# Kernel optimization log

Measured on AMD Instinct MI355X. Metric: run time of the kernel, lower is better.

## Reference

```python
import jax, jax.numpy as jnp
import numpy as np

N_NODES = 100000
N_EDGES = 640000
IN_DIM = 128
# PyG SAGEConv pyramid per SageCox(num_layers=4)
DIMS = [128, 85, 56, 28, 1]  # 85=int(128*2/3), 56=int(85*2/3), 28=int(56/2)


def setup_inputs() -> dict:
    key = jax.random.key(0)
    ks = jax.random.split(key, 2 + 3 * 4)
    inp = {
        "x": jax.random.normal(ks[0], (N_NODES, IN_DIM), dtype=jnp.float32),
        "edge_index": jax.random.randint(ks[1], (2, N_EDGES), 0, N_NODES, dtype=jnp.int64),
    }
    # Per-layer params: lin_l (weight+bias, applied to aggregated neighbors),
    # lin_r (weight only, applied to root features) -- PyG SAGEConv defaults.
    for i in range(4):
        din, dout = DIMS[i], DIMS[i + 1]
        inp[f"Wl{i}"] = jax.random.normal(ks[2 + 3 * i], (din, dout), dtype=jnp.float32) * 0.05
        inp[f"bl{i}"] = jax.random.normal(ks[3 + 3 * i], (dout,), dtype=jnp.float32) * 0.05
        inp[f"Wr{i}"] = jax.random.normal(ks[4 + 3 * i], (din, dout), dtype=jnp.float32) * 0.05
    return inp


def _sage_layer(x, src, dst, Wl, bl, Wr):
    # mean aggregation of source-node features at destination nodes
    msg = x[src]                                            # [E, din] gather
    agg = jax.ops.segment_sum(msg, dst, num_segments=N_NODES)
    deg = jax.ops.segment_sum(jnp.ones((src.shape[0],), x.dtype), dst,
                              num_segments=N_NODES)
    mean = agg / jnp.maximum(deg, 1.0)[:, None]             # [N, din]
    return mean @ Wl + bl + x @ Wr                          # [N, dout]


def reference(x, edge_index, Wl0, bl0, Wr0, Wl1, bl1, Wr1, Wl2, bl2, Wr2, Wl3, bl3, Wr3):
    src, dst = edge_index[0], edge_index[1]
    params = [(Wl0, bl0, Wr0), (Wl1, bl1, Wr1), (Wl2, bl2, Wr2), (Wl3, bl3, Wr3)]
    for Wl, bl, Wr in params:
        x = _sage_layer(x, src, dst, Wl, bl, Wr)
    return x  # [N, 1] risk scores
```

## Files before the change

### kernel.cpp

```cpp
#include <hip/hip_runtime.h>


#define NNODES 100000
#define NEDGES 640000

using bf16x8 = __attribute__((ext_vector_type(8))) short;
using f32x4  = __attribute__((ext_vector_type(4))) float;

__device__ __forceinline__ unsigned short f2bf(float f) {
    union { float f; unsigned u; } v; v.f = f;
    unsigned r = v.u + 0x7fffu + ((v.u >> 16) & 1u);
    return (unsigned short)(r >> 16);
}
__device__ __forceinline__ float bf2f(unsigned b) {
    union { unsigned u; float f; } v; v.u = b << 16;
    return v.f;
}


__global__ void hist_kernel(const int* __restrict__ edst, int* __restrict__ deg, int E) {
    int i = blockIdx.x * blockDim.x + threadIdx.x;
    if (i < E) atomicAdd(&deg[edst[i]], 1);
}

__global__ void scanA_kernel(const int* __restrict__ deg, int* __restrict__ bsum, int N) {
    __shared__ int s[256];
    int i = blockIdx.x * 256 + threadIdx.x;
    s[threadIdx.x] = (i < N) ? deg[i] : 0;
    __syncthreads();
    for (int off = 128; off > 0; off >>= 1) {
        if (threadIdx.x < off) s[threadIdx.x] += s[threadIdx.x + off];
        __syncthreads();
    }
    if (threadIdx.x == 0) bsum[blockIdx.x] = s[0];
}

__global__ void scanB_kernel(const int* __restrict__ bsum, int* __restrict__ bpre, int nb) {
    __shared__ int s[512];
    int t = threadIdx.x;
    int v = (t < nb) ? bsum[t] : 0;
    s[t] = v;
    __syncthreads();
    for (int off = 1; off < 512; off <<= 1) {
        int add = (t >= off) ? s[t - off] : 0;
        __syncthreads();
        s[t] += add;
        __syncthreads();
    }
    if (t < nb) bpre[t] = s[t] - v;
}

__global__ void scanC_kernel(const int* __restrict__ deg, const int* __restrict__ bpre,
                             int* __restrict__ rowptr, int* __restrict__ cursor, int N, int E) {
    __shared__ int s[256];
    int t = threadIdx.x;
    int i = blockIdx.x * 256 + t;
    int v = (i < N) ? deg[i] : 0;
    s[t] = v;
    __syncthreads();
    for (int off = 1; off < 256; off <<= 1) {
        int add = (t >= off) ? s[t - off] : 0;
        __syncthreads();
        s[t] += add;
        __syncthreads();
    }
    if (i < N) {
        int excl = bpre[blockIdx.x] + s[t] - v;
        rowptr[i] = excl;
        cursor[i] = excl;
        if (i == N - 1) rowptr[N] = E;
    }
}

__global__ void fill_kernel(const int* __restrict__ esrc, const int* __restrict__ edst,
                            int* __restrict__ cursor, int* __restrict__ csr, int E) {
    int i = blockIdx.x * blockDim.x + threadIdx.x;
    if (i < E) {
        int pos = atomicAdd(&cursor[edst[i]], 1);
        csr[pos] = esrc[i];
    }
}


__device__ __forceinline__ void packT_one(const float* Wl, const float* Wr,
                                          unsigned short* WcT, int idx, int DIN,
                                          int KP, int DOUT, int DOUTP) {
    int c = idx / KP, k = idx - c * KP;
    float v = 0.0f;
    if (k < DIN) {
        if (c < DOUT) v = Wl[k * DOUT + c];
        else if (c >= DOUTP && c < DOUTP + DOUT) v = Wr[k * DOUT + (c - DOUTP)];
    }
    WcT[idx] = f2bf(v);
}

__global__ void packAll_kernel(const float* __restrict__ Wl0, const float* __restrict__ Wr0,
                               const float* __restrict__ Wl1, const float* __restrict__ Wr1,
                               const float* __restrict__ Wl2, const float* __restrict__ Wr2,
                               unsigned short* __restrict__ Wc0,
                               unsigned short* __restrict__ Wc1,
                               unsigned short* __restrict__ Wc2) {
    const int S0 = 176 * 128, S1 = 112 * 96, S2 = 64 * 64;
    int idx = blockIdx.x * blockDim.x + threadIdx.x;
    if (idx < S0) packT_one(Wl0, Wr0, Wc0, idx, 128, 128, 85, 85);
    else if (idx < S0 + S1) packT_one(Wl1, Wr1, Wc1, idx - S0, 85, 96, 56, 56);
    else if (idx < S0 + S1 + S2) packT_one(Wl2, Wr2, Wc2, idx - S0 - S1, 56, 64, 28, 28);
}


template <bool XFP32, int KP, int SIN, int NTILES, int DOUT, int DOUTP, int SPP, int SACC>
__global__ void __launch_bounds__(256)
projm_kernel(const void* __restrict__ xin,
             const unsigned short* __restrict__ WcT,
             const float* __restrict__ bl,
             unsigned short* __restrict__ p,
             unsigned short* __restrict__ acc_out, int N) {
    constexpr int KT = KP / 32;
    const int lane = threadIdx.x & 63;
    const int wave = threadIdx.x >> 6;
    const int l15 = lane & 15;
    const int lk  = lane >> 4;

    const int row0 = (blockIdx.x * 4 + wave) * 32;

    bf16x8 afrag[2][KT];
#pragma unroll
    for (int h = 0; h < 2; ++h) {
        int arow = row0 + h * 16 + l15;
        if (arow >= N) arow = N - 1;
        if constexpr (XFP32) {
            const float* xr = (const float*)xin + (size_t)arow * SIN + lk * 8;
#pragma unroll
            for (int kt = 0; kt < KT; ++kt) {
                const float4 a = *(const float4*)(xr + kt * 32);
                const float4 b = *(const float4*)(xr + kt * 32 + 4);
                bf16x8 v;
                v[0] = (short)f2bf(a.x); v[1] = (short)f2bf(a.y);
                v[2] = (short)f2bf(a.z); v[3] = (short)f2bf(a.w);
                v[4] = (short)f2bf(b.x); v[5] = (short)f2bf(b.y);
                v[6] = (short)f2bf(b.z); v[7] = (short)f2bf(b.w);
                afrag[h][kt] = v;
            }
        } else {
            const unsigned short* xr = (const unsigned short*)xin + (size_t)arow * SIN + lk * 8;
#pragma unroll
            for (int kt = 0; kt < KT; ++kt)
                afrag[h][kt] = *(const bf16x8*)(xr + kt * 32);
        }
    }

#pragma unroll 2
    for (int nt = 0; nt < NTILES; ++nt) {
        const unsigned short* wp = WcT + (size_t)(nt * 16 + l15) * KP + lk * 8;
        bf16x8 bfrag[KT];
#pragma unroll
        for (int kt = 0; kt < KT; ++kt)
            bfrag[kt] = *(const bf16x8*)(wp + kt * 32);

        f32x4 a0 = {0.f, 0.f, 0.f, 0.f};
        f32x4 a1 = {0.f, 0.f, 0.f, 0.f};
#pragma unroll
        for (int kt = 0; kt < KT; ++kt) {
            a0 = __builtin_amdgcn_mfma_f32_16x16x32_bf16(afrag[0][kt], bfrag[kt], a0, 0, 0, 0);
            a1 = __builtin_amdgcn_mfma_f32_16x16x32_bf16(afrag[1][kt], bfrag[kt], a1, 0, 0, 0);
        }

        const int col = nt * 16 + l15;
#pragma unroll
        for (int h = 0; h < 2; ++h) {
            const f32x4 a = h ? a1 : a0;
            const int rbase = row0 + h * 16 + lk * 4;
#pragma unroll
            for (int j = 0; j < 4; ++j) {
                const int row = rbase + j;
                if (row >= N) continue;
                const float v = a[j];
                if (col < DOUT) {
                    p[(size_t)row * SPP + col] = f2bf(v);
                } else if (col >= DOUTP && col < DOUTP + DOUT) {
                    const int co = col - DOUTP;
                    acc_out[(size_t)row * SACC + co] = f2bf(v + bl[co]);
                }
            }
        }
    }
}


template <int DOUT, int SP, int SN>
__global__ void __launch_bounds__(256)
gatherb_kernel(const int* __restrict__ rowptr, const int* __restrict__ csr,
               const unsigned short* __restrict__ p, const unsigned short* __restrict__ acc,
               unsigned short* __restrict__ xnext, int N) {
    const int node = __builtin_amdgcn_readfirstlane((blockIdx.x * 256 + threadIdx.x) >> 6);
    const int lane = threadIdx.x & 63;
    if (node >= N) return;
    const int beg = rowptr[node], end = rowptr[node + 1];
    const float inv = 1.0f / (float)max(end - beg, 1);
    constexpr int NPAIR = (DOUT + 1) / 2;
    const int co = 2 * lane;

    float s0 = 0.f, s1 = 0.f, s2 = 0.f, s3 = 0.f;
    float h0 = 0.f, h1 = 0.f, h2 = 0.f, h3 = 0.f;
    if (lane < NPAIR) {
        int j = beg;
        for (; j + 4 <= end; j += 4) {
            const unsigned u0 = *(const unsigned*)(p + (size_t)csr[j]     * SP + co);
            const unsigned u1 = *(const unsigned*)(p + (size_t)csr[j + 1] * SP + co);
            const unsigned u2 = *(const unsigned*)(p + (size_t)csr[j + 2] * SP + co);
            const unsigned u3 = *(const unsigned*)(p + (size_t)csr[j + 3] * SP + co);
            s0 += bf2f(u0 & 0xffffu); h0 += bf2f(u0 >> 16);
            s1 += bf2f(u1 & 0xffffu); h1 += bf2f(u1 >> 16);
            s2 += bf2f(u2 & 0xffffu); h2 += bf2f(u2 >> 16);
            s3 += bf2f(u3 & 0xffffu); h3 += bf2f(u3 >> 16);
        }
        for (; j < end; ++j) {
            const unsigned u0 = *(const unsigned*)(p + (size_t)csr[j] * SP + co);
            s0 += bf2f(u0 & 0xffffu); h0 += bf2f(u0 >> 16);
        }
    }
    if (co < SN) {
        const float slo = (s0 + s1) + (s2 + s3);
        const float shi = (h0 + h1) + (h2 + h3);
        float lo = 0.f, hi = 0.f;
        if (co < DOUT)     lo = bf2f((unsigned)acc[(size_t)node * SP + co])     + inv * slo;
        if (co + 1 < DOUT) hi = bf2f((unsigned)acc[(size_t)node * SP + co + 1]) + inv * shi;
        const unsigned w = (unsigned)f2bf(lo) | ((unsigned)f2bf(hi) << 16);
        *(unsigned*)(xnext + (size_t)node * SN + co) = w;
    }
}


__global__ void __launch_bounds__(256)
gather2g_kernel(const int* __restrict__ rowptr, const int* __restrict__ csr,
                const unsigned short* __restrict__ p, const unsigned short* __restrict__ acc,
                const float* __restrict__ Wl3, const float* __restrict__ bl3,
                const float* __restrict__ Wr3,
                float* __restrict__ p3, float* __restrict__ out, int N) {
    const int node = __builtin_amdgcn_readfirstlane((blockIdx.x * 256 + threadIdx.x) >> 6);
    const int lane = threadIdx.x & 63;
    if (node >= N) return;
    const int beg = rowptr[node], end = rowptr[node + 1];
    const float inv = 1.0f / (float)max(end - beg, 1);
    const int co = 2 * lane;

    float s0 = 0.f, s1 = 0.f, s2 = 0.f, s3 = 0.f;
    float h0 = 0.f, h1 = 0.f, h2 = 0.f, h3 = 0.f;
    if (lane < 14) {
        int j = beg;
        for (; j + 4 <= end; j += 4) {
            const unsigned u0 = *(const unsigned*)(p + (size_t)csr[j]     * 32 + co);
            const unsigned u1 = *(const unsigned*)(p + (size_t)csr[j + 1] * 32 + co);
            const unsigned u2 = *(const unsigned*)(p + (size_t)csr[j + 2] * 32 + co);
            const unsigned u3 = *(const unsigned*)(p + (size_t)csr[j + 3] * 32 + co);
            s0 += bf2f(u0 & 0xffffu); h0 += bf2f(u0 >> 16);
            s1 += bf2f(u1 & 0xffffu); h1 += bf2f(u1 >> 16);
            s2 += bf2f(u2 & 0xffffu); h2 += bf2f(u2 >> 16);
            s3 += bf2f(u3 & 0xffffu); h3 += bf2f(u3 >> 16);
        }
        for (; j < end; ++j) {
            const unsigned u0 = *(const unsigned*)(p + (size_t)csr[j] * 32 + co);
            s0 += bf2f(u0 & 0xffffu); h0 += bf2f(u0 >> 16);
        }
    }
    float xlo = 0.f, xhi = 0.f, wl0 = 0.f, wl1 = 0.f, wr0 = 0.f, wr1 = 0.f;
    if (lane < 14) {
        xlo = bf2f((unsigned)acc[(size_t)node * 32 + co])     + inv * ((s0 + s1) + (s2 + s3));
        xhi = bf2f((unsigned)acc[(size_t)node * 32 + co + 1]) + inv * ((h0 + h1) + (h2 + h3));
        wl0 = Wl3[co]; wl1 = Wl3[co + 1];
        wr0 = Wr3[co]; wr1 = Wr3[co + 1];
    }
    float sl = xlo * wl0 + xhi * wl1;
    float sr = xlo * wr0 + xhi * wr1;
#pragma unroll
    for (int off = 32; off > 0; off >>= 1) {
        sl += __shfl_xor(sl, off, 64);
        sr += __shfl_xor(sr, off, 64);
    }
    if (lane == 0) {
        p3[node] = sl;
        out[node] = sr + bl3[0];
    }
}

__global__ void gather1_kernel(const int* __restrict__ rowptr, const int* __restrict__ csr,
                               const float* __restrict__ p, float* __restrict__ out, int N) {
    const int node = blockIdx.x * blockDim.x + threadIdx.x;
    if (node >= N) return;
    const int beg = rowptr[node], end = rowptr[node + 1];
    const float inv = 1.0f / (float)max(end - beg, 1);
    float a0 = 0.f, a1 = 0.f, a2 = 0.f, a3 = 0.f;
    int j = beg;
    for (; j + 4 <= end; j += 4) {
        a0 += p[csr[j]]; a1 += p[csr[j + 1]]; a2 += p[csr[j + 2]]; a3 += p[csr[j + 3]];
    }
    for (; j < end; ++j) a0 += p[csr[j]];
    out[node] += inv * ((a0 + a1) + (a2 + a3));
}


extern "C" void kernel_launch(void* const* d_in, const int* in_sizes, int n_in,
                              void* d_out, int out_size, void* d_ws, size_t ws_size,
                              hipStream_t stream) {
    const float* x  = (const float*)d_in[0];
    const int*   ei = (const int*)d_in[1];
    const int N = NNODES;
    const int E = NEDGES;
    const int* esrc = ei;
    const int* edst = ei + E;

    const float* Wl[4] = {(const float*)d_in[2], (const float*)d_in[5],
                          (const float*)d_in[8], (const float*)d_in[11]};
    const float* bl[4] = {(const float*)d_in[3], (const float*)d_in[6],
                          (const float*)d_in[9], (const float*)d_in[12]};
    const float* Wr[4] = {(const float*)d_in[4], (const float*)d_in[7],
                          (const float*)d_in[10], (const float*)d_in[13]};

    char* base = (char*)d_ws;
    size_t off = 0;
    auto alloc = [&](size_t bytes) {
        char* r = base + off;
        off += (bytes + 255) & ~(size_t)255;
        return r;
    };
    unsigned short* pB   = (unsigned short*)alloc((size_t)N * 96 * 2);
    unsigned short* accB = (unsigned short*)alloc((size_t)N * 96 * 2);
    unsigned short* xp   = (unsigned short*)alloc((size_t)N * 96 * 2);
    float*          p3   = (float*)alloc((size_t)N * 4);
    unsigned short* Wc0  = (unsigned short*)alloc((size_t)176 * 128 * 2);
    unsigned short* Wc1  = (unsigned short*)alloc((size_t)112 * 96 * 2);
    unsigned short* Wc2  = (unsigned short*)alloc((size_t)64 * 64 * 2);
    int* degi   = (int*)alloc((size_t)N * 4);
    int* rowptr = (int*)alloc((size_t)(N + 1) * 4);
    int* cursor = (int*)alloc((size_t)N * 4);
    int* csr    = (int*)alloc((size_t)E * 4);
    int* bsum   = (int*)alloc(512 * 4);
    int* bpre   = (int*)alloc(512 * 4);

    unsigned short* x2 = xp;

    const int nb = (N + 255) / 256;

    hipMemsetAsync(degi, 0, (size_t)N * sizeof(int), stream);
    hist_kernel<<<(E + 255) / 256, 256, 0, stream>>>(edst, degi, E);
    scanA_kernel<<<nb, 256, 0, stream>>>(degi, bsum, N);
    scanB_kernel<<<1, 512, 0, stream>>>(bsum, bpre, nb);
    scanC_kernel<<<nb, 256, 0, stream>>>(degi, bpre, rowptr, cursor, N, E);
    fill_kernel<<<(E + 255) / 256, 256, 0, stream>>>(esrc, edst, cursor, csr, E);

    const int packTot = 176 * 128 + 112 * 96 + 64 * 64;
    packAll_kernel<<<(packTot + 255) / 256, 256, 0, stream>>>(
        Wl[0], Wr[0], Wl[1], Wr[1], Wl[2], Wr[2], Wc0, Wc1, Wc2);

    const int projBlocks = (N + 127) / 128;

    projm_kernel<true, 128, 128, 11, 85, 85, 96, 96><<<projBlocks, 256, 0, stream>>>(
        x, Wc0, bl[0], pB, accB, N);
    gatherb_kernel<85, 96, 96><<<(N + 3) / 4, 256, 0, stream>>>(
        rowptr, csr, pB, accB, xp, N);

    projm_kernel<false, 96, 96, 7, 56, 56, 64, 64><<<projBlocks, 256, 0, stream>>>(
        xp, Wc1, bl[1], pB, accB, N);
    gatherb_kernel<56, 64, 64><<<(N + 3) / 4, 256, 0, stream>>>(
        rowptr, csr, pB, accB, x2, N);

    projm_kernel<false, 64, 64, 4, 28, 28, 32, 32><<<projBlocks, 256, 0, stream>>>(
        x2, Wc2, bl[2], pB, accB, N);

    gather2g_kernel<<<(N + 3) / 4, 256, 0, stream>>>(
        rowptr, csr, pB, accB, Wl[3], bl[3], Wr[3], p3, (float*)d_out, N);
    gather1_kernel<<<(N + 255) / 256, 256, 0, stream>>>(
        rowptr, csr, p3, (float*)d_out, N);
}
```

Baseline: 268.5 us.

## Stage weights and outputs through LDS for coalesced projection stores

The projection kernel now copies the packed weight matrix into shared memory once per block and reads MFMA B-fragments from there instead of global memory. Output tiles are written to an LDS staging buffer and then stored with 16-byte vectorized, fully coalesced writes, replacing scattered 2-byte per-element stores. The weight packing is padded so the Wl and Wr halves each fill exactly SPP columns, and padded columns now receive zeros. This adds LDS usage and extra block barriers, which may lower occupancy.

```diff
diff --git a/kernel.cpp b/kernel.cpp
--- a/kernel.cpp
+++ b/kernel.cpp
@@ -100,33 +100,48 @@
                                unsigned short* __restrict__ Wc0,
                                unsigned short* __restrict__ Wc1,
                                unsigned short* __restrict__ Wc2) {
-    const int S0 = 176 * 128, S1 = 112 * 96, S2 = 64 * 64;
+    const int S0 = 192 * 128, S1 = 128 * 96, S2 = 64 * 64;
     int idx = blockIdx.x * blockDim.x + threadIdx.x;
-    if (idx < S0) packT_one(Wl0, Wr0, Wc0, idx, 128, 128, 85, 85);
-    else if (idx < S0 + S1) packT_one(Wl1, Wr1, Wc1, idx - S0, 85, 96, 56, 56);
-    else if (idx < S0 + S1 + S2) packT_one(Wl2, Wr2, Wc2, idx - S0 - S1, 56, 64, 28, 28);
-}
-
-
-template <bool XFP32, int KP, int SIN, int NTILES, int DOUT, int DOUTP, int SPP, int SACC>
+    if (idx < S0) packT_one(Wl0, Wr0, Wc0, idx, 128, 128, 85, 96);
+    else if (idx < S0 + S1) packT_one(Wl1, Wr1, Wc1, idx - S0, 85, 96, 56, 64);
+    else if (idx < S0 + S1 + S2) packT_one(Wl2, Wr2, Wc2, idx - S0 - S1, 56, 64, 28, 32);
+}
+
+
+template <bool XFP32, int KP, int SIN, int NTILES, int DOUT, int SPP>
 __global__ void __launch_bounds__(256)
 projm_kernel(const void* __restrict__ xin,
              const unsigned short* __restrict__ WcT,
              const float* __restrict__ bl,
              unsigned short* __restrict__ p,
              unsigned short* __restrict__ acc_out, int N) {
-    constexpr int KT = KP / 32;
+    constexpr int KT   = KP / 32;
+    constexpr int HT   = NTILES / 2;
+    constexpr int CW   = NTILES * 16;
+    constexpr int WSTR = KP + 8;
+    constexpr int LSTR = SPP + 8;
+    static_assert(HT * 16 == SPP, "phase width must equal SPP");
+    __shared__ short wS[CW * WSTR];
+    __shared__ short oS[128 * LSTR];
+
     const int lane = threadIdx.x & 63;
     const int wave = threadIdx.x >> 6;
     const int l15 = lane & 15;
     const int lk  = lane >> 4;
-
-    const int row0 = (blockIdx.x * 4 + wave) * 32;
+    const int row0 = blockIdx.x * 128;
+    const int wrow = wave * 32;
+
+    for (int c8 = threadIdx.x; c8 < CW * (KP / 8); c8 += 256) {
+        const int c  = c8 / (KP / 8);
+        const int k8 = c8 - c * (KP / 8);
+        *(bf16x8*)(wS + c * WSTR + k8 * 8) =
+            *(const bf16x8*)(WcT + (size_t)c * KP + k8 * 8);
+    }
 
     bf16x8 afrag[2][KT];
 #pragma unroll
     for (int h = 0; h < 2; ++h) {
-        int arow = row0 + h * 16 + l15;
+        int arow = row0 + wrow + h * 16 + l15;
         if (arow >= N) arow = N - 1;
         if constexpr (XFP32) {
             const float* xr = (const float*)xin + (size_t)arow * SIN + lk * 8;
@@ -149,40 +164,52 @@
         }
     }
 
+    __syncthreads();
+
+    const int rows_here = min(128, N - row0);
+    const int cnt8 = rows_here * (SPP / 8);
+
+#pragma unroll
+    for (int ph = 0; ph < 2; ++ph) {
 #pragma unroll 2
-    for (int nt = 0; nt < NTILES; ++nt) {
-        const unsigned short* wp = WcT + (size_t)(nt * 16 + l15) * KP + lk * 8;
-        bf16x8 bfrag[KT];
-#pragma unroll
-        for (int kt = 0; kt < KT; ++kt)
-            bfrag[kt] = *(const bf16x8*)(wp + kt * 32);
-
-        f32x4 a0 = {0.f, 0.f, 0.f, 0.f};
-        f32x4 a1 = {0.f, 0.f, 0.f, 0.f};
-#pragma unroll
-        for (int kt = 0; kt < KT; ++kt) {
-            a0 = __builtin_amdgcn_mfma_f32_16x16x32_bf16(afrag[0][kt], bfrag[kt], a0, 0, 0, 0);
-            a1 = __builtin_amdgcn_mfma_f32_16x16x32_bf16(afrag[1][kt], bfrag[kt], a1, 0, 0, 0);
-        }
-
-        const int col = nt * 16 + l15;
-#pragma unroll
-        for (int h = 0; h < 2; ++h) {
-            const f32x4 a = h ? a1 : a0;
-            const int rbase = row0 + h * 16 + lk * 4;
-#pragma unroll
-            for (int j = 0; j < 4; ++j) {
-                const int row = rbase + j;
-                if (row >= N) continue;
-                const float v = a[j];
-                if (col < DOUT) {
-                    p[(size_t)row * SPP + col] = f2bf(v);
-                } else if (col >= DOUTP && col < DOUTP + DOUT) {
-                    const int co = col - DOUTP;
-                    acc_out[(size_t)row * SACC + co] = f2bf(v + bl[co]);
-                }
+        for (int nt = 0; nt < HT; ++nt) {
+            const short* wp = wS + (size_t)((ph * HT + nt) * 16 + l15) * WSTR + lk * 8;
+            bf16x8 bfrag[KT];
+#pragma unroll
+            for (int kt = 0; kt < KT; ++kt)
+                bfrag[kt] = *(const bf16x8*)(wp + kt * 32);
+
+            f32x4 a0 = {0.f, 0.f, 0.f, 0.f};
+            f32x4 a1 = {0.f, 0.f, 0.f, 0.f};
+#pragma unroll
+            for (int kt = 0; kt < KT; ++kt) {
+                a0 = __builtin_amdgcn_mfma_f32_16x16x32_bf16(afrag[0][kt], bfrag[kt], a0, 0, 0, 0);
+                a1 = __builtin_amdgcn_mfma_f32_16x16x32_bf16(afrag[1][kt], bfrag[kt], a1, 0, 0, 0);
             }
-        }
+
+            const int co = nt * 16 + l15;
+            const float bias = (ph == 1 && co < DOUT) ? bl[co] : 0.0f;
+#pragma unroll
+            for (int h = 0; h < 2; ++h) {
+                const f32x4 a = h ? a1 : a0;
+                const int rl = wrow + h * 16 + lk * 4;
+#pragma unroll
+                for (int j = 0; j < 4; ++j)
+                    oS[(rl + j) * LSTR + co] = (short)f2bf(a[j] + bias);
+            }
+        }
+
+        __syncthreads();
+
+        unsigned short* dst = ph ? acc_out : p;
+        for (int e8 = threadIdx.x; e8 < cnt8; e8 += 256) {
+            const int row = e8 / (SPP / 8);
+            const int c8  = e8 - row * (SPP / 8);
+            *(bf16x8*)(dst + (size_t)row0 * SPP + (size_t)e8 * 8) =
+                *(const bf16x8*)(oS + row * LSTR + c8 * 8);
+        }
+
+        __syncthreads();
     }
 }
 
@@ -327,8 +354,8 @@
     unsigned short* accB = (unsigned short*)alloc((size_t)N * 96 * 2);
     unsigned short* xp   = (unsigned short*)alloc((size_t)N * 96 * 2);
     float*          p3   = (float*)alloc((size_t)N * 4);
-    unsigned short* Wc0  = (unsigned short*)alloc((size_t)176 * 128 * 2);
-    unsigned short* Wc1  = (unsigned short*)alloc((size_t)112 * 96 * 2);
+    unsigned short* Wc0  = (unsigned short*)alloc((size_t)192 * 128 * 2);
+    unsigned short* Wc1  = (unsigned short*)alloc((size_t)128 * 96 * 2);
     unsigned short* Wc2  = (unsigned short*)alloc((size_t)64 * 64 * 2);
     int* degi   = (int*)alloc((size_t)N * 4);
     int* rowptr = (int*)alloc((size_t)(N + 1) * 4);
@@ -348,23 +375,23 @@
     scanC_kernel<<<nb, 256, 0, stream>>>(degi, bpre, rowptr, cursor, N, E);
     fill_kernel<<<(E + 255) / 256, 256, 0, stream>>>(esrc, edst, cursor, csr, E);
 
-    const int packTot = 176 * 128 + 112 * 96 + 64 * 64;
+    const int packTot = 192 * 128 + 128 * 96 + 64 * 64;
     packAll_kernel<<<(packTot + 255) / 256, 256, 0, stream>>>(
         Wl[0], Wr[0], Wl[1], Wr[1], Wl[2], Wr[2], Wc0, Wc1, Wc2);
 
     const int projBlocks = (N + 127) / 128;
 
-    projm_kernel<true, 128, 128, 11, 85, 85, 96, 96><<<projBlocks, 256, 0, stream>>>(
+    projm_kernel<true, 128, 128, 12, 85, 96><<<projBlocks, 256, 0, stream>>>(
         x, Wc0, bl[0], pB, accB, N);
     gatherb_kernel<85, 96, 96><<<(N + 3) / 4, 256, 0, stream>>>(
         rowptr, csr, pB, accB, xp, N);
 
-    projm_kernel<false, 96, 96, 7, 56, 56, 64, 64><<<projBlocks, 256, 0, stream>>>(
+    projm_kernel<false, 96, 96, 8, 56, 64><<<projBlocks, 256, 0, stream>>>(
         xp, Wc1, bl[1], pB, accB, N);
     gatherb_kernel<56, 64, 64><<<(N + 3) / 4, 256, 0, stream>>>(
         rowptr, csr, pB, accB, x2, N);
 
-    projm_kernel<false, 64, 64, 4, 28, 28, 32, 32><<<projBlocks, 256, 0, stream>>>(
+    projm_kernel<false, 64, 64, 4, 28, 32><<<projBlocks, 256, 0, stream>>>(
         x2, Wc2, bl[2], pB, accB, N);
 
     gather2g_kernel<<<(N + 3) / 4, 256, 0, stream>>>(
```

Result: faster. 254.9 us (-5.1%).
